# Performance work log

Measured on AMD Instinct MI355X. Metric: run time of the kernel, lower is better.

Reference implementation:

```python
import math
import jax, jax.numpy as jnp
import numpy as np

SAMPLE_RATIO = 0.25
K_NN = 5


def grid_index(loc_orig, H, W):
    # loc in [-1,1] -> nearest grid cell index (row-major)
    loc = jnp.clip(loc_orig, -1.0, 1.0) * 0.5 + 0.5
    ix = jnp.clip(jnp.round(loc[..., 0] * (W - 1)).astype(jnp.int32), 0, W - 1)
    iy = jnp.clip(jnp.round(loc[..., 1] * (H - 1)).astype(jnp.int32), 0, H - 1)
    return iy * W + ix  # [B, N0]


def token2map(x, loc_orig, idx_agg, H, W):
    # scatter token features (replicated to original points) into HxW grid, cell-average
    B, N, C = x.shape
    N0 = idx_agg.shape[1]
    idx_hw = grid_index(loc_orig, H, W)
    off = jnp.arange(B, dtype=jnp.int32)[:, None]
    idx_hw_flat = (idx_hw + off * (H * W)).reshape(-1)
    value = jnp.ones((B * N0,), x.dtype)
    all_w = jax.ops.segment_sum(value, idx_hw_flat, num_segments=B * H * W) + 1e-6
    value = value / all_w[idx_hw_flat]
    x_src = jnp.take_along_axis(x, idx_agg[..., None], axis=1).reshape(B * N0, C)
    x_map = jax.ops.segment_sum(x_src * value[:, None], idx_hw_flat, num_segments=B * H * W)
    return x_map.reshape(B, H, W, C).transpose(0, 3, 1, 2)  # [B,C,H,W]


def map2token(x_map, N, loc_orig, idx_agg, agg_weight):
    # gather grid features back to tokens, weighted by per-token-normalized agg_weight
    B, C, H, W = x_map.shape
    N0 = idx_agg.shape[1]
    idx_hw = grid_index(loc_orig, H, W)
    off = jnp.arange(B, dtype=jnp.int32)[:, None]
    idx_tok_flat = (idx_agg + off * N).reshape(-1)
    idx_hw_flat = (idx_hw + off * (H * W)).reshape(-1)
    value = agg_weight.reshape(-1).astype(x_map.dtype)
    all_w = jax.ops.segment_sum(value, idx_tok_flat, num_segments=B * N) + 1e-6
    value = value / all_w[idx_tok_flat]
    feat = x_map.transpose(0, 2, 3, 1).reshape(B * H * W, C)[idx_hw_flat]
    out = jax.ops.segment_sum(feat * value[:, None], idx_tok_flat, num_segments=B * N)
    return out.reshape(B, N, C)


def cluster_dpc_knn(x, Ns, k):
    # DPC-KNN clustering (no_grad in original -> stop_gradient)
    B, N, C = x.shape
    x = jax.lax.stop_gradient(x)
    x2 = jnp.sum(x * x, axis=-1)
    d2 = x2[:, :, None] + x2[:, None, :] - 2.0 * jnp.einsum('bic,bjc->bij', x, x)
    dist = jnp.sqrt(jnp.maximum(d2, 0.0)) / jnp.sqrt(jnp.asarray(C, x.dtype))
    dist_nearest = -jax.lax.top_k(-dist, k)[0]                 # k smallest dists (incl self)
    density = jnp.exp(-jnp.mean(dist_nearest ** 2, axis=-1))    # [B,N]
    # deterministic tiny tie-break noise (original uses torch.rand*1e-6)
    density = density + jax.random.uniform(jax.random.key(42), density.shape, density.dtype) * 1e-6
    mask = (density[:, None, :] > density[:, :, None]).astype(x.dtype)
    dist_max = jnp.max(dist.reshape(B, -1), axis=-1)[:, None, None]
    dist_ind = jnp.min(dist * mask + dist_max * (1.0 - mask), axis=-1)
    score = dist_ind * density
    index_down = jax.lax.top_k(score, Ns)[1]                    # [B,Ns] cluster centers
    dist_c = jnp.take_along_axis(dist, index_down[:, :, None], axis=1)  # [B,Ns,N]
    idx_cluster = jnp.argmin(dist_c, axis=1).astype(jnp.int32)  # [B,N]
    # centers belong to their own cluster
    flat = (index_down + jnp.arange(B)[:, None] * N).reshape(-1)
    own = jnp.tile(jnp.arange(Ns, dtype=jnp.int32), B)
    idx_cluster = idx_cluster.reshape(-1).at[flat].set(own).reshape(B, N)
    return idx_cluster


def merge_tokens(x, idx_cluster, Ns, weight, idx_agg):
    # weighted average of tokens per cluster; propagate mapping/weights to original points
    B, N, C = x.shape
    idx = (idx_cluster + jnp.arange(B, dtype=jnp.int32)[:, None] * Ns).reshape(-1)
    w = weight.reshape(-1)
    all_w = jax.ops.segment_sum(w, idx, num_segments=B * Ns) + 1e-6
    nw = w / all_w[idx]
    x_merged = jax.ops.segment_sum(x.reshape(B * N, C) * nw[:, None], idx,
                                   num_segments=B * Ns).reshape(B, Ns, C)
    norm_weight = nw.reshape(B, N, 1)
    idx_agg_new = jnp.take_along_axis(idx_cluster, idx_agg, axis=1)          # [B,N0]
    weight_t = jnp.take_along_axis(norm_weight, idx_agg[..., None], axis=1)  # [B,N0,1]
    return x_merged, idx_agg_new, weight_t


def ctm_forward(x, loc_orig, idx_agg, agg_weight, conv_w, conv_b, skip_w, ln_g, ln_b,
                conf_w, conf_b, H, W):
    B, N, C = x.shape
    x_map = token2map(x, loc_orig, idx_agg, H, W)
    x_map = jax.lax.conv_general_dilated(
        x_map, conv_w, window_strides=(2, 2), padding=((1, 1), (1, 1)),
        dimension_numbers=('NCHW', 'OIHW', 'NCHW')) + conv_b[None, :, None, None]
    xt = map2token(x_map, N, loc_orig, idx_agg, agg_weight) + x @ skip_w.T
    mu = jnp.mean(xt, axis=-1, keepdims=True)
    var = jnp.mean((xt - mu) ** 2, axis=-1, keepdims=True)
    xt = (xt - mu) / jnp.sqrt(var + 1e-5) * ln_g + ln_b
    conf = xt @ conf_w.T + conf_b          # [B,N,1]
    weight = jnp.exp(conf)
    Ns = max(math.ceil(N * SAMPLE_RATIO), 1)
    idx_cluster = cluster_dpc_knn(xt, Ns, K_NN)
    x_down, idx_agg_down, weight_t = merge_tokens(xt, idx_cluster, Ns, weight, idx_agg)
    agg_weight_down = agg_weight * weight_t
    agg_weight_down = agg_weight_down / jnp.max(agg_weight_down, axis=1, keepdims=True)
    # down_block is identity in this reference
    return x_down, idx_agg_down, agg_weight_down


def setup_inputs() -> dict:
    key = jax.random.key(0)
    ks = jax.random.split(key, 10)
    B, N, C, C2, H, W = 4, 3136, 64, 128, 56, 56
    return {
        'x': jax.random.normal(ks[0], (B, N, C), jnp.float32),
        'loc_orig': jax.random.normal(ks[1], (B, N, 2), jnp.float32),
        'idx_agg': jax.random.randint(ks[2], (B, N), 0, N),
        'agg_weight': jax.random.uniform(ks[3], (B, N, 1), jnp.float32, 0.1, 1.0),
        'conv_w': jax.random.normal(ks[4], (C2, C, 3, 3), jnp.float32) * 0.02,
        'conv_b': jnp.zeros((C2,), jnp.float32),
        'skip_w': jax.random.normal(ks[5], (C2, C), jnp.float32) * 0.02,
        'ln_g': jnp.ones((C2,), jnp.float32),
        'ln_b': jnp.zeros((C2,), jnp.float32),
        'conf_w': jax.random.normal(ks[6], (1, C2), jnp.float32) * 0.02,
        'conf_b': jnp.zeros((1,), jnp.float32),
        'H': 56,
        'W': 56,
    }


def reference(x, loc_orig, idx_agg, agg_weight, conv_w, conv_b, skip_w, ln_g, ln_b,
              conf_w, conf_b, H, W):
    return ctm_forward(x, loc_orig, idx_agg, agg_weight, conv_w, conv_b, skip_w,
                       ln_g, ln_b, conf_w, conf_b, H, W)
```

## Files before the change

kernel.cpp:

```cpp
#include <hip/hip_runtime.h>
#include <math.h>
#include <float.h>

#define Bq   4
#define Nq   3136
#define Cq   64
#define C2q  128
#define Hq   56
#define Wq   56
#define HWq  (Hq*Wq)
#define HOq  28
#define WOq  28
#define HWOq (HOq*WOq)
#define NSq  784
#define KNN  5
#define BNq  (Bq*Nq)

#define T64   64
#define KC    32
#define NIT64 (Nq/T64)
#define NT_C  ((NSq+T64-1)/T64)
#define NSPL  8
#define NSPA  2
#define LDP   34
// ... 71 lines not shown
    for (int i = 0; i < 5; i++) {
        const int* rot = (i % 2 == 0) ? R0 : R1;
        #pragma unroll
        for (int r = 0; r < 4; r++) { x0 += x1; x1 = rotl32(x1, rot[r]); x1 ^= x0; }
        x0 += ks[(i + 1) % 3];
        x1 += ks[(i + 2) % 3] + (u32)(i + 1);
    }
    u32 bits = lo ? x0 : x1;
    u32 fb = (bits >> 9) | 0x3f800000u;
    float f; __builtin_memcpy(&f, &fb, 4);
    return f - 1.0f;
}

static __device__ __forceinline__ int gridIndex(float lx, float ly, int Wd, int Hd) {
    double x = fmin(fmax((double)lx, -1.0), 1.0) * 0.5 + 0.5;
    double y = fmin(fmax((double)ly, -1.0), 1.0) * 0.5 + 0.5;
    int ix = (int)rint(x * (double)(Wd - 1)); ix = min(max(ix, 0), Wd - 1);
    int iy = (int)rint(y * (double)(Hd - 1)); iy = min(max(iy, 0), Hd - 1);
    return iy * Wd + ix;
}

__global__ void ctm_fallback(float* out, int n) {
    int t = blockIdx.x * blockDim.x + threadIdx.x;
    if (t < n) out[t] = 0.0f;
}

__global__ void ctm_prep(const float* __restrict__ loc, const int* __restrict__ idx_agg,
                         const float* __restrict__ aggw,
                         int* cell56, int* cell28, int* cnt56, double* allwtok) {
    int t = blockIdx.x * blockDim.x + threadIdx.x;
    if (t >= BNq) return;
    int b = t / Nq;
    float lx = loc[2 * t], ly = loc[2 * t + 1];
    int c56 = gridIndex(lx, ly, Wq, Hq);
    int c28 = gridIndex(lx, ly, WOq, HOq);
    cell56[t] = c56; cell28[t] = c28;
    atomicAdd(&cnt56[b * HWq + c56], 1);
    int tok = clampTok(idx_agg[t]);
    atomicAdd(&allwtok[b * Nq + tok], (double)aggw[t]);
}

__global__ void ctm_t2m(const float* __restrict__ x, const int* __restrict__ idx_agg,
                        const int* __restrict__ cell56, const int* __restrict__ cnt56,
                        double* xmap56T) {
    int id = blockIdx.x * blockDim.x + threadIdx.x;
    if (id >= BNq * Cq) return;
    int t = id / Cq, c = id - t * Cq;
    int b = t / Nq;
    int cell = cell56[t];
    double v = 1.0 / ((double)cnt56[b * HWq + cell] + 1e-6);
    double xv = (double)x[(size_t)(b * Nq + clampTok(idx_agg[t])) * Cq + c];
    atomicAdd(&xmap56T[((size_t)b * HWq + cell) * Cq + c], xv * v);
}

__global__ void ctm_wt(const float* __restrict__ w, float* wT) {
    int id = blockIdx.x * blockDim.x + threadIdx.x;
    if (id >= C2q * Cq * 9) return;
    int co = id & (C2q - 1);
    int rem = id >> 7;
    int tap = rem % 9;
    int ci = rem / 9;
    wT[id] = w[(size_t)co * Cq * 9 + ci * 9 + tap];
}

__global__ __launch_bounds__(256)
void ctm_conv(const double* __restrict__ xmap56T, const float* __restrict__ wT,
              const float* __restrict__ bias, double* xmap28T) {
    __shared__ double sIn[2][9][Cq];
    int blk = blockIdx.x;
    int b  = blk & (Bq - 1);
    int cp = blk >> 2;
    int tid = threadIdx.x;
    int co = tid & (C2q - 1);
    int cl = tid >> 7;
    const double* xb = xmap56T + (size_t)b * HWq * Cq;
    for (int idx = tid; idx < 2 * 9 * Cq; idx += 256) {
        int cell_l = idx / (9 * Cq);
        int rem = idx - cell_l * (9 * Cq);
        int tap = rem >> 6;
        int ci  = rem & 63;
        int cell = 2 * cp + cell_l;
        int ox = cell % WOq, oy = cell / WOq;
        int ky = tap / 3, kx = tap - ky * 3;
        int iy = 2 * oy + ky - 1, ix = 2 * ox + kx - 1;
        double v = 0.0;
        if (iy >= 0 && iy < Hq && ix >= 0 && ix < Wq)
            v = xb[(size_t)(iy * Wq + ix) * Cq + ci];
        sIn[cell_l][tap][ci] = v;
    }
    __syncthreads();
    double acc = (double)bias[co];
    for (int ci = 0; ci < Cq; ci++) {
        #pragma unroll
        for (int tap = 0; tap < 9; tap++)
            acc += sIn[cl][tap][ci] * (double)wT[(size_t)(ci * 9 + tap) * C2q + co];
    }
    int cell = 2 * cp + cl;
    xmap28T[((size_t)b * HWOq + cell) * C2q + co] = acc;
}

__global__ void ctm_m2t(const double* __restrict__ xmap28T, const float* __restrict__ aggw,
                        const int* __restrict__ idx_agg, const int* __restrict__ cell28,
                        const double* __restrict__ allwtok, double* xt) {
    int id = blockIdx.x * blockDim.x + threadIdx.x;
    if (id >= BNq * C2q) return;
    int t = id / C2q, c = id - t * C2q;
    int b = t / Nq;
    int tok = clampTok(idx_agg[t]);
    double v = (double)aggw[t] / (allwtok[b * Nq + tok] + 1e-6);
    double f = xmap28T[((size_t)b * HWOq + cell28[t]) * C2q + c];
    atomicAdd(&xt[(size_t)(b * Nq + tok) * C2q + c], f * v);
}

__global__ __launch_bounds__(C2q)
void ctm_finalize(double* xt, const float* __restrict__ x, const float* __restrict__ skipw,
                  const float* __restrict__ lng, const float* __restrict__ lnb,
                  const float* __restrict__ confw, const float* __restrict__ confb,
                  double* x2o, double* weightv) {
    int bn = blockIdx.x; int c = threadIdx.x;
    double* row = xt + (size_t)bn * C2q;
    const float* xr = x + (size_t)bn * Cq;
    double acc = row[c];
    const float* sw = skipw + c * Cq;
    #pragma unroll 16
    for (int k = 0; k < Cq; k++) acc += (double)xr[k] * (double)sw[k];
    __shared__ double red[C2q];
    __shared__ double stat[2];
    red[c] = acc; __syncthreads();
    for (int off = C2q / 2; off > 0; off >>= 1) { if (c < off) red[c] += red[c + off]; __syncthreads(); }
    if (c == 0) stat[0] = red[0] * (1.0 / C2q);
    __syncthreads();
    double mu = stat[0];
    double d = acc - mu;
    red[c] = d * d; __syncthreads();
    for (int off = C2q / 2; off > 0; off >>= 1) { if (c < off) red[c] += red[c + off]; __syncthreads(); }
    if (c == 0) stat[1] = red[0] * (1.0 / C2q);
    __syncthreads();
    double var = stat[1];
    double v = d / sqrt(var + 1e-5) * (double)lng[c] + (double)lnb[c];
    row[c] = v;
    red[c] = v * v; __syncthreads();
    for (int off = C2q / 2; off > 0; off >>= 1) { if (c < off) red[c] += red[c + off]; __syncthreads(); }
    if (c == 0) x2o[bn] = red[0];
    __syncthreads();
    red[c] = v * (double)confw[c]; __syncthreads();
    for (int off = C2q / 2; off > 0; off >>= 1) { if (c < off) red[c] += red[c + off]; __syncthreads(); }
    if (c == 0) weightv[bn] = exp(red[0] + (double)confb[0]);
}


__global__ __launch_bounds__(256, 2)
void ctm_pass1(const double* __restrict__ xt, const double* __restrict__ x2,
               double* pbest, double* pmax) {
    __shared__ double sA[T64][LDP];
    __shared__ double sB[T64][LDP];
    __shared__ double sx2j[T64];
    int blk = blockIdx.x;
    int b  = blk & (Bq - 1);
    int s  = (blk >> 2) & (NSPL - 1);
    int it = blk >> 5;
    int tid = threadIdx.x;
    const double* xtb = xt + (size_t)b * Nq * C2q;
    const double* x2b = x2 + (size_t)b * Nq;
    int i0 = it * T64;
    int jt_beg = c_spl[s], jt_end = c_spl[s + 1];

    int wv = tid >> 6, ln = tid & 63;
    int l15 = ln & 15, l4 = ln >> 4;
    int mode = mfma_mode_probe(l4, l15);

    if (mode < 2) {
        int rw[4];
        #pragma unroll
        for (int v = 0; v < 4; v++) rw[v] = (mode == 0) ? (4 * l4 + v) : (l4 + 4 * v);
        int rbase = i0 + wv * 16;
        double x2i[4];
        #pragma unroll
        for (int v = 0; v < 4; v++) x2i[v] = x2b[rbase + rw[v]];
        double best[4][KNN]; double mx[4];
        #pragma unroll
        for (int v = 0; v < 4; v++) {
            mx[v] = -DBL_MAX;
            #pragma unroll
            for (int k = 0; k < KNN; k++) best[v][k] = DBL_MAX;
        }
        for (int jt = jt_beg; jt < jt_end; jt++) {
            int j0 = jt * T64;
            d64x4 acc[4];
            #pragma unroll
            for (int bc = 0; bc < 4; bc++)
                #pragma unroll
                for (int v = 0; v < 4; v++) acc[bc][v] = 0.0;
            for (int kc = 0; kc < 4; kc++) {
                __syncthreads();
                #pragma unroll
                for (int idx = tid; idx < T64 * KC / 2; idx += 256) {
                    int r = idx >> 4, c = (idx & 15) * 2;
                    *(double2*)&sA[r][c] = *(const double2*)&xtb[(size_t)(i0 + r) * C2q + kc * KC + c];
                    *(double2*)&sB[r][c] = *(const double2*)&xtb[(size_t)(j0 + r) * C2q + kc * KC + c];
                }
                if (kc == 0 && tid < T64) sx2j[tid] = x2b[j0 + tid];
                __syncthreads();
                #pragma unroll
                for (int st = 0; st < 8; st++) {
                    double av = sA[wv * 16 + l15][4 * st + l4];
                    #pragma unroll
                    for (int bc = 0; bc < 4; bc++) {
                        double bv = sB[bc * 16 + l15][4 * st + l4];
                        acc[bc] = __builtin_amdgcn_mfma_f64_16x16x4f64(av, bv, acc[bc], 0, 0, 0);
                    }
                }
            }
            #pragma unroll
            for (int bc = 0; bc < 4; bc++) {
                double xj = sx2j[bc * 16 + l15];
                #pragma unroll
                for (int v = 0; v < 4; v++) {
                    double d2 = x2i[v] + xj - 2.0 * acc[bc][v];
                    mx[v] = fmax(mx[v], d2);
                    ins5(best[v], d2);
                }
            }
        }
        for (int m = 1; m <= 8; m <<= 1) {
            #pragma unroll
            for (int v = 0; v < 4; v++) {
                double p[KNN];
                #pragma unroll
                for (int k = 0; k < KNN; k++) p[k] = __shfl_xor(best[v][k], m);
                mx[v] = fmax(mx[v], __shfl_xor(mx[v], m));
                merge5(best[v], p);
            }
        }
        if (l15 == 0) {
            #pragma unroll
            for (int v = 0; v < 4; v++) {
                int gi = b * Nq + rbase + rw[v];
                size_t base = ((size_t)s * BNq + gi) * KNN;
                #pragma unroll
                for (int k = 0; k < KNN; k++) pbest[base + k] = best[v][k];
                pmax[(size_t)s * BNq + gi] = mx[v];
            }
        }
    } else {
        int tx = tid & 15, ty = tid >> 4;
        double x2i[4];
        #pragma unroll
        for (int r = 0; r < 4; r++) x2i[r] = x2b[i0 + ty + 16 * r];
        double best[4][KNN]; double mx[4];
        #pragma unroll
        for (int r = 0; r < 4; r++) {
            mx[r] = -DBL_MAX;
            #pragma unroll
            for (int k = 0; k < KNN; k++) best[r][k] = DBL_MAX;
        }
        for (int jt = jt_beg; jt < jt_end; jt++) {
            int j0 = jt * T64;
            double acc[4][4];
            #pragma unroll
            for (int r = 0; r < 4; r++)
                #pragma unroll
                for (int q = 0; q < 4; q++) acc[r][q] = 0.0;
            for (int kc = 0; kc < 4; kc++) {
                __syncthreads();
                #pragma unroll
                for (int idx = tid; idx < T64 * KC / 2; idx += 256) {
                    int r = idx >> 4, c = (idx & 15) * 2;
                    *(double2*)&sA[r][c] = *(const double2*)&xtb[(size_t)(i0 + r) * C2q + kc * KC + c];
                    *(double2*)&sB[r][c] = *(const double2*)&xtb[(size_t)(j0 + r) * C2q + kc * KC + c];
                }
                if (kc == 0 && tid < T64) sx2j[tid] = x2b[j0 + tid];
                __syncthreads();
                #pragma unroll 4
                for (int cc = 0; cc < KC; cc += 2) {
                    double2 xi[4], xj[4];
                    #pragma unroll
                    for (int r = 0; r < 4; r++) xi[r] = *(const double2*)&sA[ty + 16 * r][cc];
                    #pragma unroll
                    for (int q = 0; q < 4; q++) xj[q] = *(const double2*)&sB[tx + 16 * q][cc];
                    #pragma unroll
                    for (int r = 0; r < 4; r++)
                        #pragma unroll
                        for (int q = 0; q < 4; q++) acc[r][q] += xi[r].x * xj[q].x;
                    #pragma unroll
                    for (int r = 0; r < 4; r++)
                        #pragma unroll
                        for (int q = 0; q < 4; q++) acc[r][q] += xi[r].y * xj[q].y;
                }
            }
            #pragma unroll
            for (int r = 0; r < 4; r++)
                #pragma unroll
                for (int q = 0; q < 4; q++) {
                    double d2 = x2i[r] + sx2j[tx + 16 * q] - 2.0 * acc[r][q];
                    mx[r] = fmax(mx[r], d2);
                    ins5(best[r], d2);
                }
        }
        for (int m = 1; m <= 8; m <<= 1) {
            #pragma unroll
            for (int r = 0; r < 4; r++) {
                double p[KNN];
                #pragma unroll
                for (int k = 0; k < KNN; k++) p[k] = __shfl_xor(best[r][k], m);
                mx[r] = fmax(mx[r], __shfl_xor(mx[r], m));
                merge5(best[r], p);
            }
        }
        if (tx == 0) {
            #pragma unroll
            for (int r = 0; r < 4; r++) {
                int gi = b * Nq + i0 + ty + 16 * r;
                size_t base = ((size_t)s * BNq + gi) * KNN;
                #pragma unroll
                for (int k = 0; k < KNN; k++) pbest[base + k] = best[r][k];
                pmax[(size_t)s * BNq + gi] = mx[r];
            }
        }
    }
}

__global__ void ctm_merge1(const double* __restrict__ pbest, const double* __restrict__ pmax,
                           double* density, double* maxd2) {
    int t = blockIdx.x * blockDim.x + threadIdx.x;
    if (t >= BNq) return;
    double a[KNN];
    #pragma unroll
    for (int k = 0; k < KNN; k++) a[k] = pbest[(size_t)t * KNN + k];
    double mxv = pmax[t];
    #pragma unroll
    for (int s = 1; s < NSPL; s++) {
        double p[KNN];
        #pragma unroll
        for (int k = 0; k < KNN; k++) p[k] = pbest[((size_t)s * BNq + t) * KNN + k];
        merge5(a, p);
        mxv = fmax(mxv, pmax[(size_t)s * BNq + t]);
    }
    double sum = 0.0;
    #pragma unroll
    for (int k = 0; k < KNN; k++) sum += fmax(a[k], 0.0);
    density[t] = exp(-sum / (double)(C2q * KNN)) + (double)(tf_uniform(t) * 1e-6f);
    atomicMaxPosD(&maxd2[t / Nq], mxv);
}

__global__ __launch_bounds__(256, 2)
void ctm_pass2(const double* __restrict__ xt, const double* __restrict__ x2,
               const double* __restrict__ density, double* pmin) {
    __shared__ double sA[T64][LDP];
    __shared__ double sB[T64][LDP];
    __shared__ double sx2j[T64];
    __shared__ double sdj[T64];
    int blk = blockIdx.x;
    int b  = blk & (Bq - 1);
    int s  = (blk >> 2) & (NSPL - 1);
    int it = blk >> 5;
    int tid = threadIdx.x;
    const double* xtb = xt + (size_t)b * Nq * C2q;
    const double* x2b = x2 + (size_t)b * Nq;
    const double* db  = density + (size_t)b * Nq;
    int i0 = it * T64;
    int jt_beg = c_spl[s], jt_end = c_spl[s + 1];

    int wv = tid >> 6, ln = tid & 63;
    int l15 = ln & 15, l4 = ln >> 4;
    int mode = mfma_mode_probe(l4, l15);

    if (mode < 2) {
        int rw[4];
        #pragma unroll
        for (int v = 0; v < 4; v++) rw[v] = (mode == 0) ? (4 * l4 + v) : (l4 + 4 * v);
        int rbase = i0 + wv * 16;
        double x2i[4], di[4], mn[4];
        #pragma unroll
        for (int v = 0; v < 4; v++) {
            x2i[v] = x2b[rbase + rw[v]];
            di[v]  = db[rbase + rw[v]];
            mn[v]  = DBL_MAX;
        }
        for (int jt = jt_beg; jt < jt_end; jt++) {
            int j0 = jt * T64;
            d64x4 acc[4];
            #pragma unroll
            for (int bc = 0; bc < 4; bc++)
                #pragma unroll
                for (int v = 0; v < 4; v++) acc[bc][v] = 0.0;
            for (int kc = 0; kc < 4; kc++) {
                __syncthreads();
                #pragma unroll
                for (int idx = tid; idx < T64 * KC / 2; idx += 256) {
                    int r = idx >> 4, c = (idx & 15) * 2;
                    *(double2*)&sA[r][c] = *(const double2*)&xtb[(size_t)(i0 + r) * C2q + kc * KC + c];
                    *(double2*)&sB[r][c] = *(const double2*)&xtb[(size_t)(j0 + r) * C2q + kc * KC + c];
                }
                if (kc == 0 && tid < T64) { sx2j[tid] = x2b[j0 + tid]; sdj[tid] = db[j0 + tid]; }
                __syncthreads();
                #pragma unroll
                for (int st = 0; st < 8; st++) {
                    double av = sA[wv * 16 + l15][4 * st + l4];
                    #pragma unroll
                    for (int bc = 0; bc < 4; bc++) {
                        double bv = sB[bc * 16 + l15][4 * st + l4];
                        acc[bc] = __builtin_amdgcn_mfma_f64_16x16x4f64(av, bv, acc[bc], 0, 0, 0);
                    }
                }
            }
            #pragma unroll
            for (int bc = 0; bc < 4; bc++) {
                double xj = sx2j[bc * 16 + l15];
                double dj = sdj[bc * 16 + l15];
                #pragma unroll
                for (int v = 0; v < 4; v++) {
                    double d2 = x2i[v] + xj - 2.0 * acc[bc][v];
                    if (dj > di[v]) mn[v] = fmin(mn[v], d2);
                }
            }
        }
        for (int m = 1; m <= 8; m <<= 1) {
            #pragma unroll
            for (int v = 0; v < 4; v++) mn[v] = fmin(mn[v], __shfl_xor(mn[v], m));
        }
        if (l15 == 0) {
            #pragma unroll
            for (int v = 0; v < 4; v++) {
                int gi = b * Nq + rbase + rw[v];
                pmin[(size_t)s * BNq + gi] = mn[v];
            }
        }
    } else {
        int tx = tid & 15, ty = tid >> 4;
        double x2i[4], di[4], mn[4];
        #pragma unroll
        for (int r = 0; r < 4; r++) {
            x2i[r] = x2b[i0 + ty + 16 * r];
            di[r]  = db[i0 + ty + 16 * r];
            mn[r]  = DBL_MAX;
        }
        for (int jt = jt_beg; jt < jt_end; jt++) {
            int j0 = jt * T64;
            double acc[4][4];
            #pragma unroll
            for (int r = 0; r < 4; r++)
                #pragma unroll
                for (int q = 0; q < 4; q++) acc[r][q] = 0.0;
            for (int kc = 0; kc < 4; kc++) {
                __syncthreads();
                #pragma unroll
                for (int idx = tid; idx < T64 * KC / 2; idx += 256) {
                    int r = idx >> 4, c = (idx & 15) * 2;
                    *(double2*)&sA[r][c] = *(const double2*)&xtb[(size_t)(i0 + r) * C2q + kc * KC + c];
                    *(double2*)&sB[r][c] = *(const double2*)&xtb[(size_t)(j0 + r) * C2q + kc * KC + c];
                }
                if (kc == 0 && tid < T64) { sx2j[tid] = x2b[j0 + tid]; sdj[tid] = db[j0 + tid]; }
                __syncthreads();
                #pragma unroll 4
                for (int cc = 0; cc < KC; cc += 2) {
                    double2 xi[4], xj[4];
                    #pragma unroll
                    for (int r = 0; r < 4; r++) xi[r] = *(const double2*)&sA[ty + 16 * r][cc];
                    #pragma unroll
                    for (int q = 0; q < 4; q++) xj[q] = *(const double2*)&sB[tx + 16 * q][cc];
                    #pragma unroll
                    for (int r = 0; r < 4; r++)
                        #pragma unroll
                        for (int q = 0; q < 4; q++) acc[r][q] += xi[r].x * xj[q].x;
                    #pragma unroll
                    for (int r = 0; r < 4; r++)
                        #pragma unroll
                        for (int q = 0; q < 4; q++) acc[r][q] += xi[r].y * xj[q].y;
                }
            }
            #pragma unroll
            for (int r = 0; r < 4; r++)
                #pragma unroll
                for (int q = 0; q < 4; q++) {
                    double d2 = x2i[r] + sx2j[tx + 16 * q] - 2.0 * acc[r][q];
                    if (sdj[tx + 16 * q] > di[r]) mn[r] = fmin(mn[r], d2);
                }
        }
        for (int m = 1; m <= 8; m <<= 1) {
            #pragma unroll
            for (int r = 0; r < 4; r++) mn[r] = fmin(mn[r], __shfl_xor(mn[r], m));
        }
        if (tx == 0) {
            #pragma unroll
            for (int r = 0; r < 4; r++) {
                int gi = b * Nq + i0 + ty + 16 * r;
                pmin[(size_t)s * BNq + gi] = mn[r];
            }
        }
    }
}

__global__ void ctm_merge2(const double* __restrict__ pmin, const double* __restrict__ maxd2,
                           const double* __restrict__ density, double* score) {
    int t = blockIdx.x * blockDim.x + threadIdx.x;
    if (t >= BNq) return;
    int b = t / Nq;
    double m = pmin[t];
    #pragma unroll
    for (int s = 1; s < NSPL; s++) m = fmin(m, pmin[(size_t)s * BNq + t]);
    double mm = fmin(maxd2[b], m);
    score[t] = sqrt(fmax(mm, 0.0)) / sqrt((double)C2q) * density[t];
}

__global__ __launch_bounds__(1024)
void ctm_sort(const double* __restrict__ score, int* index_down) {
    __shared__ double s[4096];
    __shared__ int   si[4096];
    int b = blockIdx.x, tid = threadIdx.x;
    for (int i = tid; i < 4096; i += 1024) {
        if (i < Nq) {
            double v = score[b * Nq + i];
            s[i] = isnan(v) ? -DBL_MAX : v;
            si[i] = i;
        } else { s[i] = -DBL_MAX; si[i] = 0x7fffffff; }
    }
    __syncthreads();
    for (int k = 2; k <= 4096; k <<= 1) {
        for (int j = k >> 1; j > 0; j >>= 1) {
            for (int i = tid; i < 4096; i += 1024) {
                int ixj = i ^ j;
                if (ixj > i) {
                    double s1 = s[i], s2 = s[ixj];
                    int i1 = si[i], i2 = si[ixj];
                    bool before_ij = (s1 > s2) || (s1 == s2 && i1 < i2);
                    bool before_ji = (s2 > s1) || (s2 == s1 && i2 < i1);
                    bool doswap = ((i & k) == 0) ? before_ji : before_ij;
                    if (doswap) { s[i] = s2; s[ixj] = s1; si[i] = i2; si[ixj] = i1; }
                }
            }
            __syncthreads();
        }
    }
    for (int t = tid; t < NSq; t += 1024) {
        int v = si[t];
        index_down[b * NSq + t] = ((unsigned)v < (unsigned)Nq) ? v : 0;
    }
}

__global__ __launch_bounds__(256, 2)
void ctm_assign(const double* __restrict__ xt, const double* __restrict__ x2,
                const int* __restrict__ index_down, double* pbd, int* pbs) {
    __shared__ double sA[T64][LDP];
    __shared__ double sB[T64][LDP];
    __shared__ double sx2c[T64];
    __shared__ int    sidx[T64];
    int blk = blockIdx.x;
    int b  = blk & (Bq - 1);
    int s  = (blk >> 2) & (NSPA - 1);
    int it = blk >> 3;
    int tid = threadIdx.x;
    const double* xtb = xt + (size_t)b * Nq * C2q;
    const double* x2b = x2 + (size_t)b * Nq;
    int i0 = it * T64;
    int jt_beg = c_spla[s], jt_end = c_spla[s + 1];

    int wv = tid >> 6, ln = tid & 63;
    int l15 = ln & 15, l4 = ln >> 4;
    int mode = mfma_mode_probe(l4, l15);

    if (mode < 2) {
        int rw[4];
        #pragma unroll
        for (int v = 0; v < 4; v++) rw[v] = (mode == 0) ? (4 * l4 + v) : (l4 + 4 * v);
        int rbase = i0 + wv * 16;
        double x2i[4], bd[4];
        int bs[4];
        #pragma unroll
        for (int v = 0; v < 4; v++) { x2i[v] = x2b[rbase + rw[v]]; bd[v] = DBL_MAX; bs[v] = NSq - 1; }
        for (int jt = jt_beg; jt < jt_end; jt++) {
            int j0 = jt * T64;
            __syncthreads();
            if (tid < T64) {
                int j = index_down[b * NSq + min(j0 + tid, NSq - 1)];
                sidx[tid] = j;
                sx2c[tid] = x2b[j];
            }
            __syncthreads();
            d64x4 acc[4];
            #pragma unroll
            for (int bc = 0; bc < 4; bc++)
                #pragma unroll
                for (int v = 0; v < 4; v++) acc[bc][v] = 0.0;
            for (int kc = 0; kc < 4; kc++) {
                if (kc) __syncthreads();
                #pragma unroll
                for (int idx = tid; idx < T64 * KC / 2; idx += 256) {
                    int r = idx >> 4, c = (idx & 15) * 2;
                    *(double2*)&sA[r][c] = *(const double2*)&xtb[(size_t)(i0 + r) * C2q + kc * KC + c];
                    *(double2*)&sB[r][c] = *(const double2*)&xtb[(size_t)sidx[r] * C2q + kc * KC + c];
                }
                __syncthreads();
                #pragma unroll
                for (int st = 0; st < 8; st++) {
                    double av = sA[wv * 16 + l15][4 * st + l4];
                    #pragma unroll
                    for (int bc = 0; bc < 4; bc++) {
                        double bv = sB[bc * 16 + l15][4 * st + l4];
                        acc[bc] = __builtin_amdgcn_mfma_f64_16x16x4f64(av, bv, acc[bc], 0, 0, 0);
                    }
                }
            }
            #pragma unroll
            for (int bc = 0; bc < 4; bc++) {
                int sc = j0 + bc * 16 + l15;
                double xc = sx2c[bc * 16 + l15];
                #pragma unroll
                for (int v = 0; v < 4; v++) {
                    double d = fmax(x2i[v] + xc - 2.0 * acc[bc][v], 0.0);
                    if (sc < NSq && (d < bd[v] || (d == bd[v] && sc < bs[v]))) { bd[v] = d; bs[v] = sc; }
                }
            }
        }
        for (int m = 1; m <= 8; m <<= 1) {
            #pragma unroll
            for (int v = 0; v < 4; v++) {
                double pd = __shfl_xor(bd[v], m);
                int    ps = __shfl_xor(bs[v], m);
                if (pd < bd[v] || (pd == bd[v] && ps < bs[v])) { bd[v] = pd; bs[v] = ps; }
            }
        }
        if (l15 == 0) {
            #pragma unroll
            for (int v = 0; v < 4; v++) {
                int gi = b * Nq + rbase + rw[v];
                pbd[(size_t)s * BNq + gi] = bd[v];
                pbs[(size_t)s * BNq + gi] = bs[v];
            }
        }
    } else {
        int tx = tid & 15, ty = tid >> 4;
        double x2i[4], bd[4];
        int bs[4];
        #pragma unroll
        for (int r = 0; r < 4; r++) { x2i[r] = x2b[i0 + ty + 16 * r]; bd[r] = DBL_MAX; bs[r] = NSq - 1; }
        for (int jt = jt_beg; jt < jt_end; jt++) {
            int j0 = jt * T64;
            __syncthreads();
            if (tid < T64) {
                int j = index_down[b * NSq + min(j0 + tid, NSq - 1)];
                sidx[tid] = j;
                sx2c[tid] = x2b[j];
            }
            __syncthreads();
            double acc[4][4];
            #pragma unroll
            for (int r = 0; r < 4; r++)
                #pragma unroll
                for (int q = 0; q < 4; q++) acc[r][q] = 0.0;
            for (int kc = 0; kc < 4; kc++) {
                if (kc) __syncthreads();
                #pragma unroll
                for (int idx = tid; idx < T64 * KC / 2; idx += 256) {
                    int r = idx >> 4, c = (idx & 15) * 2;
                    *(double2*)&sA[r][c] = *(const double2*)&xtb[(size_t)(i0 + r) * C2q + kc * KC + c];
                    *(double2*)&sB[r][c] = *(const double2*)&xtb[(size_t)sidx[r] * C2q + kc * KC + c];
                }
                __syncthreads();
                #pragma unroll 4
                for (int cc = 0; cc < KC; cc += 2) {
                    double2 xi[4], xj[4];
                    #pragma unroll
                    for (int r = 0; r < 4; r++) xi[r] = *(const double2*)&sA[ty + 16 * r][cc];
                    #pragma unroll
                    for (int q = 0; q < 4; q++) xj[q] = *(const double2*)&sB[tx + 16 * q][cc];
                    #pragma unroll
                    for (int r = 0; r < 4; r++)
                        #pragma unroll
                        for (int q = 0; q < 4; q++) acc[r][q] += xi[r].x * xj[q].x;
                    #pragma unroll
                    for (int r = 0; r < 4; r++)
                        #pragma unroll
                        for (int q = 0; q < 4; q++) acc[r][q] += xi[r].y * xj[q].y;
                }
            }
            #pragma unroll
            for (int r = 0; r < 4; r++)
                #pragma unroll
                for (int q = 0; q < 4; q++) {
                    int sc = j0 + tx + 16 * q;
                    double d = fmax(x2i[r] + sx2c[tx + 16 * q] - 2.0 * acc[r][q], 0.0);
                    if (sc < NSq && (d < bd[r] || (d == bd[r] && sc < bs[r]))) { bd[r] = d; bs[r] = sc; }
                }
        }
        for (int m = 1; m <= 8; m <<= 1) {
            #pragma unroll
            for (int r = 0; r < 4; r++) {
                double pd = __shfl_xor(bd[r], m);
                int    ps = __shfl_xor(bs[r], m);
                if (pd < bd[r] || (pd == bd[r] && ps < bs[r])) { bd[r] = pd; bs[r] = ps; }
            }
        }
        if (tx == 0) {
            #pragma unroll
            for (int r = 0; r < 4; r++) {
                int gi = b * Nq + i0 + ty + 16 * r;
                pbd[(size_t)s * BNq + gi] = bd[r];
                pbs[(size_t)s * BNq + gi] = bs[r];
            }
        }
    }
}

__global__ void ctm_merge3(const double* __restrict__ pbd, const int* __restrict__ pbs,
                           int* idx_cluster) {
    int t = blockIdx.x * blockDim.x + threadIdx.x;
    if (t >= BNq) return;
    double d0 = pbd[t];          int s0 = pbs[t];
    double d1 = pbd[BNq + t];    int s1 = pbs[BNq + t];
    bool take1 = (d1 < d0) || (d1 == d0 && s1 < s0);
    idx_cluster[t] = take1 ? s1 : s0;
}

__global__ void ctm_override(const int* __restrict__ index_down, int* idx_cluster) {
    int t = blockIdx.x * blockDim.x + threadIdx.x;
    if (t >= Bq * NSq) return;
    int b = t / NSq, sc = t - b * NSq;
    int j = index_down[t];
    if ((unsigned)j < (unsigned)Nq) idx_cluster[b * Nq + j] = sc;
}

__global__ void ctm_zeromerged(double* xmerged) {
    int t = blockIdx.x * blockDim.x + threadIdx.x;
    if (t < Bq * NSq * C2q) xmerged[t] = 0.0;
}

__global__ void ctm_merge_w(const int* __restrict__ idx_cluster, const double* __restrict__ weightv,
                            double* allwc) {
    int t = blockIdx.x * blockDim.x + threadIdx.x;
    if (t >= BNq) return;
    int b = t / Nq;
    int sc = min(max(idx_cluster[t], 0), NSq - 1);
    atomicAdd(&allwc[b * NSq + sc], weightv[t]);
}

__global__ void ctm_merge_x(const int* __restrict__ idx_cluster, const double* __restrict__ weightv,
                            const double* __restrict__ allwc, const double* __restrict__ xt,
                            double* nw, double* xmerged) {
    int id = blockIdx.x * blockDim.x + threadIdx.x;
    if (id >= BNq * C2q) return;
    int t = id / C2q, c = id - t * C2q;
    int b = t / Nq;
    int sc = min(max(idx_cluster[t], 0), NSq - 1);
    double nv = weightv[t] / (allwc[b * NSq + sc] + 1e-6);
    if (c == 0) nw[t] = nv;
    atomicAdd(&xmerged[((size_t)(b * NSq + sc)) * C2q + c], xt[(size_t)t * C2q + c] * nv);
}

__global__ void ctm_out0(const double* __restrict__ xmerged, float* out) {
    int t = blockIdx.x * blockDim.x + threadIdx.x;
    if (t >= Bq * NSq * C2q) return;
    out[t] = (float)xmerged[t];
}

__global__ void ctm_out12(const int* __restrict__ idx_agg, const int* __restrict__ idx_cluster,
                          const double* __restrict__ nw, const float* __restrict__ aggw,
                          float* out1, double* awd, double* maxawd) {
    int t = blockIdx.x * blockDim.x + threadIdx.x;
    if (t >= BNq) return;
    int b = t / Nq;
    int tok = clampTok(idx_agg[t]);
    int sc = idx_cluster[b * Nq + tok];
    out1[t] = (float)sc;
    double a = (double)aggw[t] * nw[b * Nq + tok];
    awd[t] = a;
    atomicMaxPosD(&maxawd[b], a);
}

__global__ void ctm_out2(const double* __restrict__ awd, const double* __restrict__ maxawd, float* out2) {
    int t = blockIdx.x * blockDim.x + threadIdx.x;
    if (t >= BNq) return;
    int b = t / Nq;
    out2[t] = (float)(awd[t] / maxawd[b]);
}

extern "C" void kernel_launch(void* const* d_in, const int* in_sizes, int n_in,
                              void* d_out, int out_size, void* d_ws, size_t ws_size,
                              hipStream_t stream) {
    const float* x     = (const float*)d_in[0];
    const float* loc   = (const float*)d_in[1];
    const int*   idxag = (const int*)  d_in[2];
    const float* aggw  = (const float*)d_in[3];
    const float* convw = (const float*)d_in[4];
// ... 79 lines not shown
```

Measured before the change: 1.265 ms.

## Keep A tile in registers and double-buffer B tiles in MFMA distance kernels

In the MFMA paths of pass1, pass2 and assign, each wave's A-row fragment is loaded once into registers (32 doubles) instead of being restaged through shared memory for every j-tile. In pass1 and pass2 the B tile is double-buffered: the next K-chunk is prefetched into registers while the current chunk's MFMAs run, which leaves one barrier per chunk instead of two. This cuts redundant global and LDS traffic and overlaps loads with compute. The cost is higher register pressure under launch_bounds(256,2), which may cause spills or lower occupancy.

Result: faster. 1.237 ms (-2.2%).

```diff
diff --git a/kernel.cpp b/kernel.cpp
--- a/kernel.cpp
+++ b/kernel.cpp
@@ -247,9 +247,8 @@
 __global__ __launch_bounds__(256, 2)
 void ctm_pass1(const double* __restrict__ xt, const double* __restrict__ x2,
                double* pbest, double* pmax) {
-    __shared__ double sA[T64][LDP];
-    __shared__ double sB[T64][LDP];
-    __shared__ double sx2j[T64];
+    __shared__ double sBB[2][T64][LDP];
+    __shared__ double sx2j[2][T64];
     int blk = blockIdx.x;
     int b  = blk & (Bq - 1);
     int s  = (blk >> 2) & (NSPL - 1);
@@ -269,6 +268,13 @@
         #pragma unroll
         for (int v = 0; v < 4; v++) rw[v] = (mode == 0) ? (4 * l4 + v) : (l4 + 4 * v);
         int rbase = i0 + wv * 16;
+        double a_reg[4][8];
+        const double* arow = xtb + (size_t)(i0 + wv * 16 + l15) * C2q + l4;
+        #pragma unroll
+        for (int kc = 0; kc < 4; kc++)
+            #pragma unroll
+            for (int st = 0; st < 8; st++)
+                a_reg[kc][st] = arow[kc * KC + 4 * st];
         double x2i[4];
         #pragma unroll
         for (int v = 0; v < 4; v++) x2i[v] = x2b[rbase + rw[v]];
@@ -279,6 +285,17 @@
             #pragma unroll
             for (int k = 0; k < KNN; k++) best[v][k] = DBL_MAX;
         }
+        {
+            int j0 = jt_beg * T64;
+            #pragma unroll
+            for (int w = 0; w < 4; w++) {
+                int idx = tid + w * 256; int r = idx >> 4, c = (idx & 15) * 2;
+                *(double2*)&sBB[0][r][c] = *(const double2*)&xtb[(size_t)(j0 + r) * C2q + c];
+            }
+            if (tid < T64) sx2j[0][tid] = x2b[j0 + tid];
+        }
+        __syncthreads();
+        int q = 0;
         for (int jt = jt_beg; jt < jt_end; jt++) {
             int j0 = jt * T64;
             d64x4 acc[4];
@@ -286,6 +303,93 @@
             for (int bc = 0; bc < 4; bc++)
                 #pragma unroll
                 for (int v = 0; v < 4; v++) acc[bc][v] = 0.0;
+            #pragma unroll
+            for (int kc = 0; kc < 4; kc++) {
+                const int cb = kc & 1, nb = cb ^ 1, nkc = (kc + 1) & 3;
+                const bool lastk = (kc == 3);
+                bool hn = !lastk || (jt + 1 < jt_end);
+                int nj0 = lastk ? j0 + T64 : j0;
+                double2 sreg[4]; double xr = 0.0;
+                if (hn) {
+                    #pragma unroll
+                    for (int w = 0; w < 4; w++) {
+                        int idx = tid + w * 256; int r = idx >> 4, c = (idx & 15) * 2;
+                        sreg[w] = *(const double2*)&xtb[(size_t)(nj0 + r) * C2q + nkc * KC + c];
+                    }
+                    if (lastk && tid < T64) xr = x2b[nj0 + tid];
+                }
+                #pragma unroll
+                for (int st = 0; st < 8; st++) {
+                    double av = a_reg[kc][st];
+                    #pragma unroll
+                    for (int bc = 0; bc < 4; bc++) {
+                        double bv = sBB[cb][bc * 16 + l15][4 * st + l4];
+                        acc[bc] = __builtin_amdgcn_mfma_f64_16x16x4f64(av, bv, acc[bc], 0, 0, 0);
+                    }
+                }
+                if (hn) {
+                    #pragma unroll
+                    for (int w = 0; w < 4; w++) {
+                        int idx = tid + w * 256; int r = idx >> 4, c = (idx & 15) * 2;
+                        *(double2*)&sBB[nb][r][c] = sreg[w];
+                    }
+                    if (lastk && tid < T64) sx2j[q ^ 1][tid] = xr;
+                }
+                __syncthreads();
+            }
+            #pragma unroll
+            for (int bc = 0; bc < 4; bc++) {
+                double xj = sx2j[q][bc * 16 + l15];
+                #pragma unroll
+                for (int v = 0; v < 4; v++) {
+                    double d2 = x2i[v] + xj - 2.0 * acc[bc][v];
+                    mx[v] = fmax(mx[v], d2);
+                    ins5(best[v], d2);
+                }
+            }
+            q ^= 1;
+        }
+        for (int m = 1; m <= 8; m <<= 1) {
+            #pragma unroll
+            for (int v = 0; v < 4; v++) {
+                double p[KNN];
+                #pragma unroll
+                for (int k = 0; k < KNN; k++) p[k] = __shfl_xor(best[v][k], m);
+                mx[v] = fmax(mx[v], __shfl_xor(mx[v], m));
+                merge5(best[v], p);
+            }
+        }
+        if (l15 == 0) {
+            #pragma unroll
+            for (int v = 0; v < 4; v++) {
+                int gi = b * Nq + rbase + rw[v];
+                size_t base = ((size_t)s * BNq + gi) * KNN;
+                #pragma unroll
+                for (int k = 0; k < KNN; k++) pbest[base + k] = best[v][k];
+                pmax[(size_t)s * BNq + gi] = mx[v];
+            }
+        }
+    } else {
+        double (*sA)[LDP] = sBB[0];
+        double (*sB)[LDP] = sBB[1];
+        int tx = tid & 15, ty = tid >> 4;
+        double x2i[4];
+        #pragma unroll
+        for (int r = 0; r < 4; r++) x2i[r] = x2b[i0 + ty + 16 * r];
+        double best[4][KNN]; double mx[4];
+        #pragma unroll
+        for (int r = 0; r < 4; r++) {
+            mx[r] = -DBL_MAX;
+            #pragma unroll
+            for (int k = 0; k < KNN; k++) best[r][k] = DBL_MAX;
+        }
+        for (int jt = jt_beg; jt < jt_end; jt++) {
+            int j0 = jt * T64;
+            double acc[4][4];
+            #pragma unroll
+            for (int r = 0; r < 4; r++)
+                #pragma unroll
+                for (int q = 0; q < 4; q++) acc[r][q] = 0.0;
             for (int kc = 0; kc < 4; kc++) {
                 __syncthreads();
                 #pragma unroll
@@ -294,77 +398,7 @@
                     *(double2*)&sA[r][c] = *(const double2*)&xtb[(size_t)(i0 + r) * C2q + kc * KC + c];
                     *(double2*)&sB[r][c] = *(const double2*)&xtb[(size_t)(j0 + r) * C2q + kc * KC + c];
                 }
-                if (kc == 0 && tid < T64) sx2j[tid] = x2b[j0 + tid];
-                __syncthreads();
-                #pragma unroll
-                for (int st = 0; st < 8; st++) {
-                    double av = sA[wv * 16 + l15][4 * st + l4];
-                    #pragma unroll
-                    for (int bc = 0; bc < 4; bc++) {
-                        double bv = sB[bc * 16 + l15][4 * st + l4];
-                        acc[bc] = __builtin_amdgcn_mfma_f64_16x16x4f64(av, bv, acc[bc], 0, 0, 0);
-                    }
-                }
-            }
-            #pragma unroll
-            for (int bc = 0; bc < 4; bc++) {
-                double xj = sx2j[bc * 16 + l15];
-                #pragma unroll
-                for (int v = 0; v < 4; v++) {
-                    double d2 = x2i[v] + xj - 2.0 * acc[bc][v];
-                    mx[v] = fmax(mx[v], d2);
-                    ins5(best[v], d2);
-                }
-            }
-        }
-        for (int m = 1; m <= 8; m <<= 1) {
-            #pragma unroll
-            for (int v = 0; v < 4; v++) {
-                double p[KNN];
-                #pragma unroll
-                for (int k = 0; k < KNN; k++) p[k] = __shfl_xor(best[v][k], m);
-                mx[v] = fmax(mx[v], __shfl_xor(mx[v], m));
-                merge5(best[v], p);
-            }
-        }
-        if (l15 == 0) {
-            #pragma unroll
-            for (int v = 0; v < 4; v++) {
-                int gi = b * Nq + rbase + rw[v];
-                size_t base = ((size_t)s * BNq + gi) * KNN;
-                #pragma unroll
-                for (int k = 0; k < KNN; k++) pbest[base + k] = best[v][k];
-                pmax[(size_t)s * BNq + gi] = mx[v];
-            }
-        }
-    } else {
-        int tx = tid & 15, ty = tid >> 4;
-        double x2i[4];
-        #pragma unroll
-        for (int r = 0; r < 4; r++) x2i[r] = x2b[i0 + ty + 16 * r];
-        double best[4][KNN]; double mx[4];
-        #pragma unroll
-        for (int r = 0; r < 4; r++) {
-            mx[r] = -DBL_MAX;
-            #pragma unroll
-            for (int k = 0; k < KNN; k++) best[r][k] = DBL_MAX;
-        }
-        for (int jt = jt_beg; jt < jt_end; jt++) {
-            int j0 = jt * T64;
-            double acc[4][4];
-            #pragma unroll
-            for (int r = 0; r < 4; r++)
-                #pragma unroll
-                for (int q = 0; q < 4; q++) acc[r][q] = 0.0;
-            for (int kc = 0; kc < 4; kc++) {
-                __syncthreads();
-                #pragma unroll
-                for (int idx = tid; idx < T64 * KC / 2; idx += 256) {
-                    int r = idx >> 4, c = (idx & 15) * 2;
-                    *(double2*)&sA[r][c] = *(const double2*)&xtb[(size_t)(i0 + r) * C2q + kc * KC + c];
-                    *(double2*)&sB[r][c] = *(const double2*)&xtb[(size_t)(j0 + r) * C2q + kc * KC + c];
-                }
-                if (kc == 0 && tid < T64) sx2j[tid] = x2b[j0 + tid];
+                if (kc == 0 && tid < T64) sx2j[0][tid] = x2b[j0 + tid];
                 __syncthreads();
                 #pragma unroll 4
                 for (int cc = 0; cc < KC; cc += 2) {
@@ -387,7 +421,7 @@
             for (int r = 0; r < 4; r++)
                 #pragma unroll
                 for (int q = 0; q < 4; q++) {
-                    double d2 = x2i[r] + sx2j[tx + 16 * q] - 2.0 * acc[r][q];
+                    double d2 = x2i[r] + sx2j[0][tx + 16 * q] - 2.0 * acc[r][q];
                     mx[r] = fmax(mx[r], d2);
                     ins5(best[r], d2);
                 }
@@ -441,10 +475,9 @@
 __global__ __launch_bounds__(256, 2)
 void ctm_pass2(const double* __restrict__ xt, const double* __restrict__ x2,
                const double* __restrict__ density, double* pmin) {
-    __shared__ double sA[T64][LDP];
-    __shared__ double sB[T64][LDP];
-    __shared__ double sx2j[T64];
-    __shared__ double sdj[T64];
+    __shared__ double sBB[2][T64][LDP];
+    __shared__ double sx2j[2][T64];
+    __shared__ double sdj[2][T64];
     int blk = blockIdx.x;
     int b  = blk & (Bq - 1);
     int s  = (blk >> 2) & (NSPL - 1);
@@ -465,6 +498,13 @@
         #pragma unroll
         for (int v = 0; v < 4; v++) rw[v] = (mode == 0) ? (4 * l4 + v) : (l4 + 4 * v);
         int rbase = i0 + wv * 16;
+        double a_reg[4][8];
+        const double* arow = xtb + (size_t)(i0 + wv * 16 + l15) * C2q + l4;
+        #pragma unroll
+        for (int kc = 0; kc < 4; kc++)
+            #pragma unroll
+            for (int st = 0; st < 8; st++)
+                a_reg[kc][st] = arow[kc * KC + 4 * st];
         double x2i[4], di[4], mn[4];
         #pragma unroll
         for (int v = 0; v < 4; v++) {
@@ -472,6 +512,17 @@
             di[v]  = db[rbase + rw[v]];
             mn[v]  = DBL_MAX;
         }
+        {
+            int j0 = jt_beg * T64;
+            #pragma unroll
+            for (int w = 0; w < 4; w++) {
+                int idx = tid + w * 256; int r = idx >> 4, c = (idx & 15) * 2;
+                *(double2*)&sBB[0][r][c] = *(const double2*)&xtb[(size_t)(j0 + r) * C2q + c];
+            }
+            if (tid < T64) { sx2j[0][tid] = x2b[j0 + tid]; sdj[0][tid] = db[j0 + tid]; }
+        }
+        __syncthreads();
+        int q = 0;
         for (int jt = jt_beg; jt < jt_end; jt++) {
             int j0 = jt * T64;
             d64x4 acc[4];
@@ -479,6 +530,81 @@
             for (int bc = 0; bc < 4; bc++)
                 #pragma unroll
                 for (int v = 0; v < 4; v++) acc[bc][v] = 0.0;
+            #pragma unroll
+            for (int kc = 0; kc < 4; kc++) {
+                const int cb = kc & 1, nb = cb ^ 1, nkc = (kc + 1) & 3;
+                const bool lastk = (kc == 3);
+                bool hn = !lastk || (jt + 1 < jt_end);
+                int nj0 = lastk ? j0 + T64 : j0;
+                double2 sreg[4]; double xr = 0.0, dr = 0.0;
+                if (hn) {
+                    #pragma unroll
+                    for (int w = 0; w < 4; w++) {
+                        int idx = tid + w * 256; int r = idx >> 4, c = (idx & 15) * 2;
+                        sreg[w] = *(const double2*)&xtb[(size_t)(nj0 + r) * C2q + nkc * KC + c];
+                    }
+                    if (lastk && tid < T64) { xr = x2b[nj0 + tid]; dr = db[nj0 + tid]; }
+                }
+                #pragma unroll
+                for (int st = 0; st < 8; st++) {
+                    double av = a_reg[kc][st];
+                    #pragma unroll
+                    for (int bc = 0; bc < 4; bc++) {
+                        double bv = sBB[cb][bc * 16 + l15][4 * st + l4];
+                        acc[bc] = __builtin_amdgcn_mfma_f64_16x16x4f64(av, bv, acc[bc], 0, 0, 0);
+                    }
+                }
+                if (hn) {
+                    #pragma unroll
+                    for (int w = 0; w < 4; w++) {
+                        int idx = tid + w * 256; int r = idx >> 4, c = (idx & 15) * 2;
+                        *(double2*)&sBB[nb][r][c] = sreg[w];
+                    }
+                    if (lastk && tid < T64) { sx2j[q ^ 1][tid] = xr; sdj[q ^ 1][tid] = dr; }
+                }
+                __syncthreads();
+            }
+            #pragma unroll
+            for (int bc = 0; bc < 4; bc++) {
+                double xj = sx2j[q][bc * 16 + l15];
+                double dj = sdj[q][bc * 16 + l15];
+                #pragma unroll
+                for (int v = 0; v < 4; v++) {
+                    double d2 = x2i[v] + xj - 2.0 * acc[bc][v];
+                    if (dj > di[v]) mn[v] = fmin(mn[v], d2);
+                }
+            }
+            q ^= 1;
+        }
+        for (int m = 1; m <= 8; m <<= 1) {
+            #pragma unroll
+            for (int v = 0; v < 4; v++) mn[v] = fmin(mn[v], __shfl_xor(mn[v], m));
+        }
+        if (l15 == 0) {
+            #pragma unroll
+            for (int v = 0; v < 4; v++) {
+                int gi = b * Nq + rbase + rw[v];
+                pmin[(size_t)s * BNq + gi] = mn[v];
+            }
+        }
+    } else {
+        double (*sA)[LDP] = sBB[0];
+        double (*sB)[LDP] = sBB[1];
+        int tx = tid & 15, ty = tid >> 4;
+        double x2i[4], di[4], mn[4];
+        #pragma unroll
+        for (int r = 0; r < 4; r++) {
+            x2i[r] = x2b[i0 + ty + 16 * r];
+            di[r]  = db[i0 + ty + 16 * r];
+            mn[r]  = DBL_MAX;
+        }
+        for (int jt = jt_beg; jt < jt_end; jt++) {
+            int j0 = jt * T64;
+            double acc[4][4];
+            #pragma unroll
+            for (int r = 0; r < 4; r++)
+                #pragma unroll
+                for (int q = 0; q < 4; q++) acc[r][q] = 0.0;
             for (int kc = 0; kc < 4; kc++) {
                 __syncthreads();
                 #pragma unroll
@@ -487,65 +613,7 @@
                     *(double2*)&sA[r][c] = *(const double2*)&xtb[(size_t)(i0 + r) * C2q + kc * KC + c];
                     *(double2*)&sB[r][c] = *(const double2*)&xtb[(size_t)(j0 + r) * C2q + kc * KC + c];
                 }
-                if (kc == 0 && tid < T64) { sx2j[tid] = x2b[j0 + tid]; sdj[tid] = db[j0 + tid]; }
-                __syncthreads();
-                #pragma unroll
-                for (int st = 0; st < 8; st++) {
-                    double av = sA[wv * 16 + l15][4 * st + l4];
-                    #pragma unroll
-                    for (int bc = 0; bc < 4; bc++) {
-                        double bv = sB[bc * 16 + l15][4 * st + l4];
-                        acc[bc] = __builtin_amdgcn_mfma_f64_16x16x4f64(av, bv, acc[bc], 0, 0, 0);
-                    }
-                }
-            }
-            #pragma unroll
-            for (int bc = 0; bc < 4; bc++) {
-                double xj = sx2j[bc * 16 + l15];
-                double dj = sdj[bc * 16 + l15];
-                #pragma unroll
-                for (int v = 0; v < 4; v++) {
-                    double d2 = x2i[v] + xj - 2.0 * acc[bc][v];
-                    if (dj > di[v]) mn[v] = fmin(mn[v], d2);
-                }
-            }
-        }
-        for (int m = 1; m <= 8; m <<= 1) {
-            #pragma unroll
-            for (int v = 0; v < 4; v++) mn[v] = fmin(mn[v], __shfl_xor(mn[v], m));
-        }
-        if (l15 == 0) {
-            #pragma unroll
-            for (int v = 0; v < 4; v++) {
-                int gi = b * Nq + rbase + rw[v];
-                pmin[(size_t)s * BNq + gi] = mn[v];
-            }
-        }
-    } else {
-        int tx = tid & 15, ty = tid >> 4;
-        double x2i[4], di[4], mn[4];
-        #pragma unroll
-        for (int r = 0; r < 4; r++) {
-            x2i[r] = x2b[i0 + ty + 16 * r];
-            di[r]  = db[i0 + ty + 16 * r];
-            mn[r]  = DBL_MAX;
-        }
-        for (int jt = jt_beg; jt < jt_end; jt++) {
-            int j0 = jt * T64;
-            double acc[4][4];
-            #pragma unroll
-            for (int r = 0; r < 4; r++)
-                #pragma unroll
-                for (int q = 0; q < 4; q++) acc[r][q] = 0.0;
-            for (int kc = 0; kc < 4; kc++) {
-                __syncthreads();
-                #pragma unroll
-                for (int idx = tid; idx < T64 * KC / 2; idx += 256) {
-                    int r = idx >> 4, c = (idx & 15) * 2;
-                    *(double2*)&sA[r][c] = *(const double2*)&xtb[(size_t)(i0 + r) * C2q + kc * KC + c];
-                    *(double2*)&sB[r][c] = *(const double2*)&xtb[(size_t)(j0 + r) * C2q + kc * KC + c];
-                }
-                if (kc == 0 && tid < T64) { sx2j[tid] = x2b[j0 + tid]; sdj[tid] = db[j0 + tid]; }
+                if (kc == 0 && tid < T64) { sx2j[0][tid] = x2b[j0 + tid]; sdj[0][tid] = db[j0 + tid]; }
                 __syncthreads();
                 #pragma unroll 4
                 for (int cc = 0; cc < KC; cc += 2) {
@@ -568,8 +636,8 @@
             for (int r = 0; r < 4; r++)
                 #pragma unroll
                 for (int q = 0; q < 4; q++) {
-                    double d2 = x2i[r] + sx2j[tx + 16 * q] - 2.0 * acc[r][q];
-                    if (sdj[tx + 16 * q] > di[r]) mn[r] = fmin(mn[r], d2);
+                    double d2 = x2i[r] + sx2j[0][tx + 16 * q] - 2.0 * acc[r][q];
+                    if (sdj[0][tx + 16 * q] > di[r]) mn[r] = fmin(mn[r], d2);
                 }
         }
         for (int m = 1; m <= 8; m <<= 1) {
@@ -636,8 +704,7 @@
 __global__ __launch_bounds__(256, 2)
 void ctm_assign(const double* __restrict__ xt, const double* __restrict__ x2,
                 const int* __restrict__ index_down, double* pbd, int* pbs) {
-    __shared__ double sA[T64][LDP];
-    __shared__ double sB[T64][LDP];
+    __shared__ double sBB[2][T64][LDP];
     __shared__ double sx2c[T64];
     __shared__ int    sidx[T64];
     int blk = blockIdx.x;
@@ -659,6 +726,13 @@
         #pragma unroll
         for (int v = 0; v < 4; v++) rw[v] = (mode == 0) ? (4 * l4 + v) : (l4 + 4 * v);
         int rbase = i0 + wv * 16;
+        double a_reg[4][8];
+        const double* arow = xtb + (size_t)(i0 + wv * 16 + l15) * C2q + l4;
+        #pragma unroll
+        for (int kc = 0; kc < 4; kc++)
+            #pragma unroll
+            for (int st = 0; st < 8; st++)
+                a_reg[kc][st] = arow[kc * KC + 4 * st];
         double x2i[4], bd[4];
         int bs[4];
         #pragma unroll
@@ -682,16 +756,15 @@
                 #pragma unroll
                 for (int idx = tid; idx < T64 * KC / 2; idx += 256) {
                     int r = idx >> 4, c = (idx & 15) * 2;
-                    *(double2*)&sA[r][c] = *(const double2*)&xtb[(size_t)(i0 + r) * C2q + kc * KC + c];
-                    *(double2*)&sB[r][c] = *(const double2*)&xtb[(size_t)sidx[r] * C2q + kc * KC + c];
+                    *(double2*)&sBB[0][r][c] = *(const double2*)&xtb[(size_t)sidx[r] * C2q + kc * KC + c];
                 }
                 __syncthreads();
                 #pragma unroll
                 for (int st = 0; st < 8; st++) {
-                    double av = sA[wv * 16 + l15][4 * st + l4];
+                    double av = a_reg[kc][st];
                     #pragma unroll
                     for (int bc = 0; bc < 4; bc++) {
-                        double bv = sB[bc * 16 + l15][4 * st + l4];
+                        double bv = sBB[0][bc * 16 + l15][4 * st + l4];
                         acc[bc] = __builtin_amdgcn_mfma_f64_16x16x4f64(av, bv, acc[bc], 0, 0, 0);
                     }
                 }
@@ -724,6 +797,8 @@
             }
         }
     } else {
+        double (*sA)[LDP] = sBB[0];
+        double (*sB)[LDP] = sBB[1];
         int tx = tid & 15, ty = tid >> 4;
         double x2i[4], bd[4];
         int bs[4];
```
